# Kernel tuning notes

Measured on AMD Instinct MI355X. Metric: run time of the kernel, lower is better.

The kernel has to match this reference:

```python
import jax, jax.numpy as jnp
import numpy as np

H, W, WS, HEADS = 112, 112, 7, 8
DIM, HID = 512, 2048


def _layernorm(x, g, b, eps=1e-5):
    mu = jnp.mean(x, axis=-1, keepdims=True)
    var = jnp.var(x, axis=-1, keepdims=True)
    return (x - mu) * jax.lax.rsqrt(var + eps) * g + b


def _cpe(x, w, b):
    # depthwise 3x3 conv positional encoding with residual; x: [B, L, C]
    B, L, C = x.shape
    img = x.reshape(B, H, W, C)
    feat = jax.lax.conv_general_dilated(
        img, w, window_strides=(1, 1), padding='SAME',
        dimension_numbers=('NHWC', 'HWIO', 'NHWC'), feature_group_count=C) + b
    return x + feat.reshape(B, L, C)


def _window_partition(x):
    # [B, H, W, C] -> [B*nW, ws*ws, C]
    B, _, _, C = x.shape
    x = x.reshape(B, H // WS, WS, W // WS, WS, C)
    x = jnp.transpose(x, (0, 1, 3, 2, 4, 5))
    return x.reshape(-1, WS * WS, C)


def _window_reverse(xw, B):
    # [B*nW, ws*ws, C] -> [B, H*W, C]
    C = xw.shape[-1]
    x = xw.reshape(B, H // WS, W // WS, WS, WS, C)
    x = jnp.transpose(x, (0, 1, 3, 2, 4, 5))
    return x.reshape(B, H * W, C)


def _attention(x, qkv_w, qkv_b, proj_w, proj_b):
    # x: [nW, N, C]; standard MHA within each window
    nW, N, C = x.shape
    d = C // HEADS
    qkv = x @ qkv_w + qkv_b                      # [nW, N, 3C]
    qkv = qkv.reshape(nW, N, 3, HEADS, d)
    q, k, v = qkv[:, :, 0], qkv[:, :, 1], qkv[:, :, 2]  # [nW, N, h, d]
    scale = d ** -0.5
    attn = jnp.einsum('wqhd,wkhd->whqk', q * scale, k)
    attn = jax.nn.softmax(attn, axis=-1)
    out = jnp.einsum('whqk,wkhd->wqhd', attn, v).reshape(nW, N, C)
    return out @ proj_w + proj_b


def setup_inputs() -> dict:
    key = jax.random.key(0)
    ks = jax.random.split(key, 16)
    s = 0.02
    return {
        'x': jax.random.normal(ks[0], (4, H * W, DIM), jnp.float32),
        'cpe0_w': jax.random.normal(ks[1], (3, 3, 1, DIM), jnp.float32) * s,
        'cpe0_b': jnp.zeros((DIM,), jnp.float32),
        'cpe1_w': jax.random.normal(ks[2], (3, 3, 1, DIM), jnp.float32) * s,
        'cpe1_b': jnp.zeros((DIM,), jnp.float32),
        'ln1_g': jnp.ones((DIM,), jnp.float32),
        'ln1_b': jnp.zeros((DIM,), jnp.float32),
        'ln2_g': jnp.ones((DIM,), jnp.float32),
        'ln2_b': jnp.zeros((DIM,), jnp.float32),
        'qkv_w': jax.random.normal(ks[3], (DIM, 3 * DIM), jnp.float32) * s,
        'qkv_b': jnp.zeros((3 * DIM,), jnp.float32),
        'attn_proj_w': jax.random.normal(ks[4], (DIM, DIM), jnp.float32) * s,
        'attn_proj_b': jnp.zeros((DIM,), jnp.float32),
        'fc1_w': jax.random.normal(ks[5], (DIM, HID), jnp.float32) * s,
        'fc1_b': jnp.zeros((HID,), jnp.float32),
        'fc2_w': jax.random.normal(ks[6], (HID, DIM), jnp.float32) * s,
        'fc2_b': jnp.zeros((DIM,), jnp.float32),
    }


def reference(x, cpe0_w, cpe0_b, cpe1_w, cpe1_b, ln1_g, ln1_b, ln2_g, ln2_b,
              qkv_w, qkv_b, attn_proj_w, attn_proj_b, fc1_w, fc1_b, fc2_w, fc2_b):
    B, L, C = x.shape
    shortcut = _cpe(x, cpe0_w, cpe0_b)                 # CPE #1 (with residual)
    h = _layernorm(shortcut, ln1_g, ln1_b)
    h = _window_partition(h.reshape(B, H, W, C))       # [B*nW, 49, C]
    h = _attention(h, qkv_w, qkv_b, attn_proj_w, attn_proj_b)
    h = _window_reverse(h, B)                          # [B, L, C]
    h = shortcut + h
    h = _cpe(h, cpe1_w, cpe1_b)                        # CPE #2 (with residual)
    m = _layernorm(h, ln2_g, ln2_b)
    m = jax.nn.gelu(m @ fc1_w + fc1_b) @ fc2_w + fc2_b
    return h + m
```

## Files before the change

### kernel.cpp

```cpp
#include <hip/hip_runtime.h>
#include <stdint.h>

#define HH 112
#define WW 112
#define CC 512
#define BB 4
#define LLEN (HH*WW)
#define NTOK (BB*LLEN)
#define NHEADS 8
#define HD 64
#define HIDDEN 2048

typedef __bf16 bf16x8 __attribute__((ext_vector_type(8)));
typedef float f32x4 __attribute__((ext_vector_type(4)));
typedef int i32x8 __attribute__((ext_vector_type(8)));
typedef long i64;

__device__ __forceinline__ unsigned short f2bf(float x) {
  uint32_t u = __float_as_uint(x);
  u += 0x7fffu + ((u >> 16) & 1u);
  return (unsigned short)(u >> 16);
}
__device__ __forceinline__ float bf2f(unsigned short h) {
  return __uint_as_float((uint32_t)h << 16);
}
__device__ __forceinline__ int cvt4_fp8(float a, float b, float c, float d) {
  int r = 0;
  r = __builtin_amdgcn_cvt_pk_fp8_f32(a, b, r, false);
  r = __builtin_amdgcn_cvt_pk_fp8_f32(c, d, r, true);
  return r;
}

__device__ __forceinline__ void gload16(const void* gptr, void* lptr) {
  __builtin_amdgcn_global_load_lds(
      (const __attribute__((address_space(1))) void*)gptr,
      (__attribute__((address_space(3))) void*)lptr,
      16, 0, 0);
}

#define WAITV3() asm volatile("s_waitcnt vmcnt(3)" ::: "memory")
#define WAITV8() asm volatile("s_waitcnt vmcnt(8)" ::: "memory")
#define WAITV0() asm volatile("s_waitcnt vmcnt(0)" ::: "memory")
#define BAR() __builtin_amdgcn_s_barrier()
#define WAITL() do { asm volatile("s_waitcnt lgkmcnt(0)" ::: "memory"); \
                     __builtin_amdgcn_sched_barrier(0); } while (0)

__global__ __launch_bounds__(256) void wtranspose8_kernel(
    const float* __restrict__ w, unsigned char* __restrict__ wt, int K, int N) {
  int idx = blockIdx.x * 256 + threadIdx.x;
  if (idx >= K * N) return;
  int n = idx / K, k = idx - n * K;
  float v = w[(size_t)k * N + n] * 32.f;
  int r = __builtin_amdgcn_cvt_pk_fp8_f32(v, v, 0, false);
  wt[idx] = (unsigned char)r;
}

template <int INBF, int OUTBF>
__global__ __launch_bounds__(256) void cpe_ln_kernel(
    const void* __restrict__ xin, const float* __restrict__ w,
    const float* __restrict__ bias, const float* __restrict__ lng,
    const float* __restrict__ lnb, void* __restrict__ outp,
    unsigned char* __restrict__ ln8) {
  const int wid = threadIdx.x >> 6;
  const int lane = threadIdx.x & 63;
  const int xx = blockIdx.x * 4 + wid;
  const int yy = blockIdx.y;
  const int bb = blockIdx.z;
  const int c = lane * 8;

  float acc[8];
  {
    float4 b0 = *(const float4*)(&bias[c]);
    float4 b1 = *(const float4*)(&bias[c + 4]);
    acc[0] = b0.x; acc[1] = b0.y; acc[2] = b0.z; acc[3] = b0.w;
    acc[4] = b1.x; acc[5] = b1.y; acc[6] = b1.z; acc[7] = b1.w;
  }
  float xv[8];

  #pragma unroll
  for (int ky = 0; ky < 3; ky++) {
    int y = yy + ky - 1;
    bool yok = (unsigned)y < (unsigned)HH;
    #pragma unroll
    for (int kx = 0; kx < 3; kx++) {
      int x2 = xx + kx - 1;
      bool ok = yok && ((unsigned)x2 < (unsigned)WW);
      float v[8];
      if (ok) {
        size_t eo = (((size_t)bb * HH + y) * WW + x2) * CC + c;
        if (INBF) {
          uint4 u = *(const uint4*)(&((const unsigned short*)xin)[eo]);
          v[0] = bf2f((unsigned short)(u.x & 0xffff)); v[1] = bf2f((unsigned short)(u.x >> 16));
          v[2] = bf2f((unsigned short)(u.y & 0xffff)); v[3] = bf2f((unsigned short)(u.y >> 16));
          v[4] = bf2f((unsigned short)(u.z & 0xffff)); v[5] = bf2f((unsigned short)(u.z >> 16));
          v[6] = bf2f((unsigned short)(u.w & 0xffff)); v[7] = bf2f((unsigned short)(u.w >> 16));
        } else {
          float4 a = *(const float4*)(&((const float*)xin)[eo]);
          float4 b = *(const float4*)(&((const float*)xin)[eo + 4]);
          v[0] = a.x; v[1] = a.y; v[2] = a.z; v[3] = a.w;
          v[4] = b.x; v[5] = b.y; v[6] = b.z; v[7] = b.w;
        }
      } else {
        #pragma unroll
        for (int e = 0; e < 8; e++) v[e] = 0.f;
      }
      if (ky == 1 && kx == 1) {
        #pragma unroll
        for (int e = 0; e < 8; e++) xv[e] = v[e];
      }
      float4 w0 = *(const float4*)(&w[(ky * 3 + kx) * CC + c]);
      float4 w1 = *(const float4*)(&w[(ky * 3 + kx) * CC + c + 4]);
      acc[0] = fmaf(v[0], w0.x, acc[0]); acc[1] = fmaf(v[1], w0.y, acc[1]);
      acc[2] = fmaf(v[2], w0.z, acc[2]); acc[3] = fmaf(v[3], w0.w, acc[3]);
      acc[4] = fmaf(v[4], w1.x, acc[4]); acc[5] = fmaf(v[5], w1.y, acc[5]);
      acc[6] = fmaf(v[6], w1.z, acc[6]); acc[7] = fmaf(v[7], w1.w, acc[7]);
    }
  }

  float r[8];
  #pragma unroll
  for (int e = 0; e < 8; e++) r[e] = xv[e] + acc[e];

  const size_t o = (((size_t)bb * HH + yy) * WW + xx) * CC + c;
  if (OUTBF) {
    uint4 pk;
    pk.x = (uint32_t)f2bf(r[0]) | ((uint32_t)f2bf(r[1]) << 16);
    pk.y = (uint32_t)f2bf(r[2]) | ((uint32_t)f2bf(r[3]) << 16);
    pk.z = (uint32_t)f2bf(r[4]) | ((uint32_t)f2bf(r[5]) << 16);
    pk.w = (uint32_t)f2bf(r[6]) | ((uint32_t)f2bf(r[7]) << 16);
    *(uint4*)(&((unsigned short*)outp)[o]) = pk;
  } else {
    float4 r0, r1;
    r0.x = r[0]; r0.y = r[1]; r0.z = r[2]; r0.w = r[3];
    r1.x = r[4]; r1.y = r[5]; r1.z = r[6]; r1.w = r[7];
    *(float4*)(&((float*)outp)[o]) = r0;
    *(float4*)(&((float*)outp)[o + 4]) = r1;
  }

  float s = 0.f, ss = 0.f;
  #pragma unroll
  for (int e = 0; e < 8; e++) { s += r[e]; ss += r[e] * r[e]; }
  #pragma unroll
  for (int of = 32; of; of >>= 1) {
    s += __shfl_xor(s, of, 64);
    ss += __shfl_xor(ss, of, 64);
  }
  float mu = s * (1.f / CC);
  float var = ss * (1.f / CC) - mu * mu;
  float rsd = rsqrtf(var + 1e-5f);
  float4 g0 = *(const float4*)(&lng[c]);
  float4 g1 = *(const float4*)(&lng[c + 4]);
  float4 b0 = *(const float4*)(&lnb[c]);
  float4 b1 = *(const float4*)(&lnb[c + 4]);
  float gv[8] = {g0.x, g0.y, g0.z, g0.w, g1.x, g1.y, g1.z, g1.w};
  float bv[8] = {b0.x, b0.y, b0.z, b0.w, b1.x, b1.y, b1.z, b1.w};
  float ov[8];
  #pragma unroll
  for (int e = 0; e < 8; e++) ov[e] = (r[e] - mu) * rsd * gv[e] + bv[e];
  uint2 pk8;
  pk8.x = (uint32_t)cvt4_fp8(ov[0], ov[1], ov[2], ov[3]);
  pk8.y = (uint32_t)cvt4_fp8(ov[4], ov[5], ov[6], ov[7]);
  *(uint2*)(&ln8[o]) = pk8;
}

#define BM 256
#define BN 128
#define BK8 64

template <int MODE, int K>
__global__ __launch_bounds__(512) void gemm8_kernel(
    const unsigned char* __restrict__ A, const unsigned char* __restrict__ BT,
    const float* __restrict__ bias, const unsigned short* __restrict__ resB,
    unsigned short* __restrict__ outB16, int M, int N) {
  __shared__ unsigned char ldsb[49152];
  int nwg = gridDim.x * gridDim.y;
  int flat = blockIdx.y * gridDim.x + blockIdx.x;
  int swz = (flat & 7) * (nwg >> 3) + (flat >> 3);
  int bx = swz % gridDim.x, by = swz / gridDim.x;
  const int bm = by * BM, bn = bx * BN;
  const int t = threadIdx.x;
  const int wid = t >> 6, lane = t & 63;
  const int wr = wid >> 1, wc = wid & 1;
  const int lr = lane & 15, g = lane >> 4;
  const int swr = (lr >> 1) & 3;
  const int rb0 = (((g >> 1)      ) ^ swr) * 16 + (g & 1) * 8;
  const int rb1 = (((g >> 1) + 2) ^ swr) * 16 + (g & 1) * 8;
  const int srow = t >> 2;
  const int scol = (((t & 3) ^ ((t >> 3) & 3)) & 3) * 16;
  const size_t arow0 = (size_t)(bm + srow) * K + scol;
  const size_t arow1 = (size_t)(bm + 128 + srow) * K + scol;
  const size_t brow  = (size_t)(bn + srow) * K + scol;
  const int ldso = wid * 1024;

#define STG8(b, kt) do { \
    gload16(&A[arow0 + (kt)], ldsb + (b) * 16384 + ldso); \
    gload16(&A[arow1 + (kt)], ldsb + (b) * 16384 + 8192 + ldso); \
    gload16(&BT[brow + (kt)], ldsb + 32768 + (b) * 8192 + ldso); } while (0)

  f32x4 acc[4][4] = {};
  constexpr int nt = K / BK8;

  STG8(0, 0);
  STG8(1, BK8);

  #pragma unroll
  for (int tile = 0; tile < nt - 1; ++tile) {
    WAITV3(); BAR();
    const unsigned char* as = ldsb + (tile & 1) * 16384;
    const unsigned char* bs = ldsb + 32768 + (tile & 1) * 8192;
    i64 af0[4], af1[4], bf0[4], bf1[4];
    #pragma unroll
    for (int i = 0; i < 4; i++) {
      const unsigned char* p = &as[(wr * 64 + i * 16 + lr) * BK8];
      af0[i] = *(const i64*)(p + rb0);
      af1[i] = *(const i64*)(p + rb1);
    }
    #pragma unroll
    for (int j = 0; j < 4; j++) {
      const unsigned char* p = &bs[(wc * 64 + j * 16 + lr) * BK8];
      bf0[j] = *(const i64*)(p + rb0);
      bf1[j] = *(const i64*)(p + rb1);
    }
    WAITL();
    BAR();
    if (tile + 2 < nt) STG8(tile & 1, (tile + 2) * BK8);
    __builtin_amdgcn_s_setprio(1);
    #pragma unroll
    for (int i = 0; i < 4; i++)
      #pragma unroll
      for (int j = 0; j < 4; j++) {
        acc[i][j] = __builtin_amdgcn_mfma_f32_16x16x32_fp8_fp8(af0[i], bf0[j], acc[i][j], 0, 0, 0);
        acc[i][j] = __builtin_amdgcn_mfma_f32_16x16x32_fp8_fp8(af1[i], bf1[j], acc[i][j], 0, 0, 0);
      }
    __builtin_amdgcn_s_setprio(0);
  }
  {
    WAITV0(); BAR();
    const unsigned char* as = ldsb + ((nt - 1) & 1) * 16384;
    const unsigned char* bs = ldsb + 32768 + ((nt - 1) & 1) * 8192;
    i64 af0[4], af1[4], bf0[4], bf1[4];
    #pragma unroll
    for (int i = 0; i < 4; i++) {
      const unsigned char* p = &as[(wr * 64 + i * 16 + lr) * BK8];
      af0[i] = *(const i64*)(p + rb0);
      af1[i] = *(const i64*)(p + rb1);
    }
    #pragma unroll
    for (int j = 0; j < 4; j++) {
      const unsigned char* p = &bs[(wc * 64 + j * 16 + lr) * BK8];
      bf0[j] = *(const i64*)(p + rb0);
      bf1[j] = *(const i64*)(p + rb1);
    }
    WAITL();
    #pragma unroll
    for (int i = 0; i < 4; i++)
      #pragma unroll
      for (int j = 0; j < 4; j++) {
        acc[i][j] = __builtin_amdgcn_mfma_f32_16x16x32_fp8_fp8(af0[i], bf0[j], acc[i][j], 0, 0, 0);
        acc[i][j] = __builtin_amdgcn_mfma_f32_16x16x32_fp8_fp8(af1[i], bf1[j], acc[i][j], 0, 0, 0);
      }
  }
#undef STG8

  {
    const float SC = 0.03125f;
    float* eps = (float*)ldsb;
    const int erow = t >> 3;
    const int ecol0 = (t & 7) * 16;
    const int wrow = wr * 16 + (lane >> 4) * 4;
    const int wcol = wc * 64 + lr;
    const int gr_base = bm + (erow >> 4) * 64 + (erow & 15);
    const int gc0 = bn + ecol0;
    float bv[16];
    #pragma unroll
    for (int c4 = 0; c4 < 4; c4++)
      *(float4*)&bv[c4 * 4] = *(const float4*)&bias[gc0 + c4 * 4];
    #pragma unroll
    for (int i = 0; i < 4; i++) {
      __syncthreads();
      #pragma unroll
      for (int j = 0; j < 4; j++)
        #pragma unroll
        for (int r = 0; r < 4; r++)
          eps[(wrow + r) * 132 + wcol + j * 16] = acc[i][j][r];
      __syncthreads();
      float vv[16];
      #pragma unroll
      for (int c4 = 0; c4 < 4; c4++)
        *(float4*)&vv[c4 * 4] = *(const float4*)&eps[erow * 132 + ecol0 + c4 * 4];
      const size_t off = (size_t)(gr_base + i * 16) * N + gc0;
      uint4 r0 = *(const uint4*)&resB[off];
      uint4 r1 = *(const uint4*)&resB[off + 8];
      unsigned short ob[16];
      const uint32_t* rp = (const uint32_t*)&r0;
      #pragma unroll
      for (int c = 0; c < 8; c++) {
        uint32_t u = rp[c >> 1];
        float rv = bf2f((unsigned short)((c & 1) ? (u >> 16) : (u & 0xffff)));
        ob[c] = f2bf(vv[c] * SC + bv[c] + rv);
      }
      const uint32_t* rp1 = (const uint32_t*)&r1;
      #pragma unroll
      for (int c = 0; c < 8; c++) {
        uint32_t u = rp1[c >> 1];
        float rv = bf2f((unsigned short)((c & 1) ? (u >> 16) : (u & 0xffff)));
        ob[8 + c] = f2bf(vv[8 + c] * SC + bv[8 + c] + rv);
      }
      *(uint4*)&outB16[off]     = *(uint4*)&ob[0];
      *(uint4*)&outB16[off + 8] = *(uint4*)&ob[8];
    }
  }
}

__device__ __forceinline__ i32x8 ld_frag128(const unsigned char* base, int row, int g, int lrm7) {
  const uint4 lo = *(const uint4*)(base + row * 128 + (((2 * g)     ^ lrm7) * 16));
  const uint4 hi = *(const uint4*)(base + row * 128 + (((2 * g + 1) ^ lrm7) * 16));
  i32x8 r;
  r[0] = lo.x; r[1] = lo.y; r[2] = lo.z; r[3] = lo.w;
  r[4] = hi.x; r[5] = hi.y; r[6] = hi.z; r[7] = hi.w;
  return r;
}

template <int MODE, int K>
__global__ __launch_bounds__(256) void gemm8mx_kernel(
    const unsigned char* __restrict__ A, const unsigned char* __restrict__ BT,
    const float* __restrict__ bias, const float* __restrict__ res,
    float* __restrict__ outF, unsigned char* __restrict__ outB8,
    int M, int N) {
  __shared__ unsigned char ldsb[65536];
  const int SCALE1 = 0x7F7F7F7F;
  int nwg = gridDim.x * gridDim.y;
  int flat = blockIdx.y * gridDim.x + blockIdx.x;
  int swz = (flat & 7) * (nwg >> 3) + (flat >> 3);
  int bx = swz % gridDim.x, by = swz / gridDim.x;
  const int bm = by * 128, bn = bx * 128;
  const int t = threadIdx.x;
  const int wid = t >> 6, lane = t & 63;
  const int wr = wid >> 1, wc = wid & 1;
  const int lr = lane & 15, g = lane >> 4, lrm7 = lane & 7;
  const int wq0 = wid * 4096;
  const int scol = (((lane & 7) ^ ((lane >> 3) & 7)) & 7) * 16;
  const size_t aB0 = (size_t)(bm + wid * 32 + ((t >> 3) & 7)) * K + scol;
  const size_t bB0 = (size_t)(bn + wid * 32 + ((t >> 3) & 7)) * K + scol;

#define STGMX(p, kt) do { \
    _Pragma("unroll") for (int q_ = 0; q_ < 4; q_++) { \
      gload16(&A[aB0 + (size_t)q_ * 8 * K + (kt)],  ldsb + (p) * 16384 + wq0 + q_ * 1024); \
      gload16(&BT[bB0 + (size_t)q_ * 8 * K + (kt)], ldsb + 32768 + (p) * 16384 + wq0 + q_ * 1024); \
    } } while (0)

  f32x4 acc[4][4] = {};
  constexpr int npt = K / 128;

  STGMX(0, 0);
  STGMX(1, 128);

  #pragma unroll
  for (int pt = 0; pt < npt - 1; ++pt) {
    WAITV8(); BAR();
    const unsigned char* as = ldsb + (pt & 1) * 16384;
    const unsigned char* bs = ldsb + 32768 + (pt & 1) * 16384;
    i32x8 af[4], bf[4];
    #pragma unroll
    for (int i = 0; i < 4; i++)
      af[i] = ld_frag128(as, wr * 64 + i * 16 + lr, g, lrm7);
    #pragma unroll
    for (int j = 0; j < 4; j++)
      bf[j] = ld_frag128(bs, wc * 64 + j * 16 + lr, g, lrm7);
    WAITL();
    BAR();
    if (pt + 2 < npt) STGMX(pt & 1, (pt + 2) * 128);
    __builtin_amdgcn_s_setprio(1);
    #pragma unroll
    for (int i = 0; i < 4; i++)
      #pragma unroll
      for (int j = 0; j < 4; j++)
        acc[i][j] = __builtin_amdgcn_mfma_scale_f32_16x16x128_f8f6f4(
            af[i], bf[j], acc[i][j], 0, 0, 0, SCALE1, 0, SCALE1);
    __builtin_amdgcn_s_setprio(0);
  }
  {
    WAITV0(); BAR();
    const unsigned char* as = ldsb + ((npt - 1) & 1) * 16384;
    const unsigned char* bs = ldsb + 32768 + ((npt - 1) & 1) * 16384;
    i32x8 af[4], bf[4];
    #pragma unroll
    for (int i = 0; i < 4; i++)
      af[i] = ld_frag128(as, wr * 64 + i * 16 + lr, g, lrm7);
    #pragma unroll
    for (int j = 0; j < 4; j++)
      bf[j] = ld_frag128(bs, wc * 64 + j * 16 + lr, g, lrm7);
    WAITL();
    #pragma unroll
    for (int i = 0; i < 4; i++)
      #pragma unroll
      for (int j = 0; j < 4; j++)
        acc[i][j] = __builtin_amdgcn_mfma_scale_f32_16x16x128_f8f6f4(
            af[i], bf[j], acc[i][j], 0, 0, 0, SCALE1, 0, SCALE1);
  }
#undef STGMX

  {
    const float SC = 0.03125f;
    float* eps = (float*)ldsb;
    const int erow = t >> 2;
    const int cb = (t & 3) * 4;
    float4 bv4[8];
    #pragma unroll
    for (int c = 0; c < 8; c++)
      bv4[c] = *(const float4*)&bias[bn + cb + c * 16];
    #pragma unroll
    for (int p = 0; p < 2; p++) {
      __syncthreads();
      if (wr == p) {
        #pragma unroll
        for (int i = 0; i < 4; i++)
          #pragma unroll
          for (int j = 0; j < 4; j++)
            #pragma unroll
            for (int r = 0; r < 4; r++)
              eps[(i * 16 + g * 4 + r) * 132 + wc * 64 + j * 16 + lr] = acc[i][j][r];
      }
      __syncthreads();
      const size_t rowoff = (size_t)(bm + p * 64 + erow) * N + bn + cb;
      #pragma unroll
      for (int c = 0; c < 8; c++) {
        float4 vv = *(const float4*)&eps[erow * 132 + cb + c * 16];
        float v0 = vv.x * SC + bv4[c].x;
        float v1 = vv.y * SC + bv4[c].y;
        float v2 = vv.z * SC + bv4[c].z;
        float v3 = vv.w * SC + bv4[c].w;
        if (MODE == 1) {
          float4 rv = *(const float4*)&res[rowoff + c * 16];
          float4 ov;
          ov.x = v0 + rv.x; ov.y = v1 + rv.y; ov.z = v2 + rv.z; ov.w = v3 + rv.w;
          *(float4*)&outF[rowoff + c * 16] = ov;
        } else if (MODE == 0) {
          *(uint32_t*)&outB8[rowoff + c * 16] = (uint32_t)cvt4_fp8(v0, v1, v2, v3);
        } else {
          float gv[4];
          float vin[4] = {v0, v1, v2, v3};
          #pragma unroll
          for (int e = 0; e < 4; e++) {
            float v = vin[e];
            float a2 = v * v;
            float w = v * fmaf(a2, -0.1029436f, -2.3024849f);
            float sg = __builtin_amdgcn_rcpf(1.f + __builtin_amdgcn_exp2f(w));
            gv[e] = v * sg;
          }
          *(uint32_t*)&outB8[rowoff + c * 16] = (uint32_t)cvt4_fp8(gv[0], gv[1], gv[2], gv[3]);
        }
      }
    }
  }
}

#define WNS8 72

__global__ __launch_bounds__(64) void attn_mfma8_kernel(
    const unsigned char* __restrict__ qkv, unsigned char* __restrict__ out) {
  __shared__ unsigned char VT[64 * WNS8];
  __shared__ unsigned char Ps[64 * WNS8];
  const int task = blockIdx.x;
  const int win = task >> 3, h = task & 7;
  const int b = win >> 8, wy = (win >> 4) & 15, wx = win & 15;
  const int lane = threadIdx.x;
  const int lr = lane & 15, g = lane >> 4;

  auto tokof = [&](int r) {
    int rr = r > 48 ? 48 : r;
    int y = rr / 7, x2 = rr - y * 7;
    return (size_t)(b * LLEN + (wy * 7 + y) * WW + wx * 7 + x2);
  };

  {
    size_t vbase = tokof(lane) * 1536 + 1024 + h * 64;
    bool valid = lane <= 48;
    #pragma unroll
    for (int c = 0; c < 4; c++) {
      uint4 v = *(const uint4*)(&qkv[vbase + c * 16]);
      const unsigned char* pv = (const unsigned char*)&v;
      #pragma unroll
      for (int e = 0; e < 16; e++)
        VT[(c * 16 + e) * WNS8 + lane] = valid ? pv[e] : (unsigned char)0;
    }
  }

  size_t tok[4];
  #pragma unroll
  for (int i2 = 0; i2 < 4; i2++) tok[i2] = tokof(i2 * 16 + lr);
  i64 Qf[4][2], Kf[4][2];
  #pragma unroll
  for (int i2 = 0; i2 < 4; i2++) {
    size_t base = tok[i2] * 1536 + h * 64 + g * 8;
    #pragma unroll
    for (int ks = 0; ks < 2; ks++) {
      Qf[i2][ks] = *(const i64*)(&qkv[base + ks * 32]);
      Kf[i2][ks] = *(const i64*)(&qkv[base + 512 + ks * 32]);
    }
  }

  f32x4 acc[4][4] = {};
  #pragma unroll
  for (int ks = 0; ks < 2; ks++)
    #pragma unroll
    for (int i2 = 0; i2 < 4; i2++)
      #pragma unroll
      for (int j = 0; j < 4; j++)
        acc[i2][j] = __builtin_amdgcn_mfma_f32_16x16x32_fp8_fp8(Kf[i2][ks], Qf[j][ks], acc[i2][j], 0, 0, 0);

  #pragma unroll
  for (int j = 0; j < 4; j++) {
    float mx = -1e30f;
    #pragma unroll
    for (int i2 = 0; i2 < 4; i2++)
      #pragma unroll
      for (int r = 0; r < 4; r++) {
        int k = 16 * i2 + 4 * g + r;
        mx = fmaxf(mx, (k <= 48) ? acc[i2][j][r] : -1e30f);
      }
    mx = fmaxf(mx, __shfl_xor(mx, 16, 64));
    mx = fmaxf(mx, __shfl_xor(mx, 32, 64));
    float p[4][4];
    float sum = 0.f;
    #pragma unroll
    for (int i2 = 0; i2 < 4; i2++)
      #pragma unroll
      for (int r = 0; r < 4; r++) {
        int k = 16 * i2 + 4 * g + r;
        float e = (k <= 48) ? __expf(0.125f * (acc[i2][j][r] - mx)) : 0.f;
        p[i2][r] = e; sum += e;
      }
    sum += __shfl_xor(sum, 16, 64);
    sum += __shfl_xor(sum, 32, 64);
    float inv = 1.f / sum;
    int q = 16 * j + lr;
    #pragma unroll
    for (int i2 = 0; i2 < 4; i2++) {
      uint32_t w = (uint32_t)cvt4_fp8(p[i2][0] * inv, p[i2][1] * inv,
                                      p[i2][2] * inv, p[i2][3] * inv);
      *(uint32_t*)(&Ps[q * WNS8 + 16 * i2 + 4 * g]) = w;
    }
  }

  __syncthreads();

  f32x4 o[4][4] = {};
  #pragma unroll
  for (int ks = 0; ks < 2; ks++) {
    i64 Pf[4], Vf[4];
    #pragma unroll
    for (int i2 = 0; i2 < 4; i2++)
      Pf[i2] = *(const i64*)(&Ps[(16 * i2 + lr) * WNS8 + ks * 32 + g * 8]);
    #pragma unroll
    for (int j = 0; j < 4; j++)
      Vf[j] = *(const i64*)(&VT[(16 * j + lr) * WNS8 + ks * 32 + g * 8]);
    #pragma unroll
    for (int i2 = 0; i2 < 4; i2++)
      #pragma unroll
      for (int j = 0; j < 4; j++)
        o[i2][j] = __builtin_amdgcn_mfma_f32_16x16x32_fp8_fp8(Pf[i2], Vf[j], o[i2][j], 0, 0, 0);
  }

  #pragma unroll
  for (int i2 = 0; i2 < 4; i2++)
    #pragma unroll
    for (int r = 0; r < 4; r++) {
      int q = 16 * i2 + 4 * g + r;
      if (q <= 48) {
        size_t obase = tokof(q) * 512 + h * 64 + lr;
        #pragma unroll
        for (int j = 0; j < 4; j++) {
          float v = o[i2][j][r];
          int rr = __builtin_amdgcn_cvt_pk_fp8_f32(v, v, 0, false);
          out[obase + 16 * j] = (unsigned char)rr;
        }
      }
    }
}

extern "C" void kernel_launch(void* const* d_in, const int* in_sizes, int n_in,
                              void* d_out, int out_size, void* d_ws, size_t ws_size,
                              hipStream_t stream) {
  const float* x      = (const float*)d_in[0];
  const float* cpe0_w = (const float*)d_in[1];
  const float* cpe0_b = (const float*)d_in[2];
  const float* cpe1_w = (const float*)d_in[3];
  const float* cpe1_b = (const float*)d_in[4];
  const float* ln1_g  = (const float*)d_in[5];
  const float* ln1_b  = (const float*)d_in[6];
  const float* ln2_g  = (const float*)d_in[7];
  const float* ln2_b  = (const float*)d_in[8];
  const float* qkv_w  = (const float*)d_in[9];
  const float* qkv_b  = (const float*)d_in[10];
  const float* proj_w = (const float*)d_in[11];
  const float* proj_b = (const float*)d_in[12];
  const float* fc1_w  = (const float*)d_in[13];
  const float* fc1_b  = (const float*)d_in[14];
  const float* fc2_w  = (const float*)d_in[15];
  const float* fc2_b  = (const float*)d_in[16];
  float* out = (float*)d_out;
  char* ws = (char*)d_ws;

  unsigned char*  qkvwT8 = (unsigned char*)(ws + 0);
  unsigned char*  projwT8 = (unsigned char*)(ws + 1048576);
  unsigned char*  fc1wT8 = (unsigned char*)(ws + 2097152);
  unsigned char*  fc2wT8 = (unsigned char*)(ws + 4194304);
  unsigned short* shortcB = (unsigned short*)(ws + 6291456);
  unsigned char*  lnb8   = (unsigned char*)(ws + 109051904);
  unsigned char*  qkvb8  = (unsigned char*)(ws + 160432128);
  unsigned char*  attnb8 = (unsigned char*)(ws + 314572800);
  unsigned char*  gelub8 = (unsigned char*)(ws + 160432128);
  float* h2 = out;

  wtranspose8_kernel<<<(512 * 1536 + 255) / 256, 256, 0, stream>>>(qkv_w, qkvwT8, 512, 1536);
  wtranspose8_kernel<<<(512 * 512 + 255) / 256, 256, 0, stream>>>(proj_w, projwT8, 512, 512);
  wtranspose8_kernel<<<(512 * 2048 + 255) / 256, 256, 0, stream>>>(fc1_w, fc1wT8, 512, 2048);
  wtranspose8_kernel<<<(2048 * 512 + 255) / 256, 256, 0, stream>>>(fc2_w, fc2wT8, 2048, 512);

  cpe_ln_kernel<0, 1><<<dim3(28, 112, BB), 256, 0, stream>>>(x, cpe0_w, cpe0_b,
      ln1_g, ln1_b, shortcB, lnb8);
  gemm8mx_kernel<0, 512><<<dim3(12, 392), 256, 0, stream>>>(lnb8, qkvwT8, qkv_b, nullptr,
      nullptr, qkvb8, NTOK, 1536);
  attn_mfma8_kernel<<<8192, 64, 0, stream>>>(qkvb8, attnb8);
  gemm8_kernel<3, 512><<<dim3(4, 196), 512, 0, stream>>>(attnb8, projwT8, proj_b,
      shortcB, shortcB, NTOK, 512);
  cpe_ln_kernel<1, 0><<<dim3(28, 112, BB), 256, 0, stream>>>(shortcB, cpe1_w, cpe1_b,
      ln2_g, ln2_b, h2, lnb8);
  gemm8mx_kernel<2, 512><<<dim3(16, 392), 256, 0, stream>>>(lnb8, fc1wT8, fc1_b, nullptr,
      nullptr, gelub8, NTOK, 2048);
  gemm8mx_kernel<1, 2048><<<dim3(4, 392), 256, 0, stream>>>(gelub8, fc2wT8, fc2_b, h2,
      out, nullptr, NTOK, 512);
}
```

Baseline: 536.0 us.

## Use eight waves per block in MX fp8 GEMM with 4x2 wave tiling

Raises the MX fp8 GEMM block from 256 to 512 threads and splits the 128x128 tile across 2x4 waves, each computing 64x32 instead of 64x64. Each thread now issues half as many async global-to-LDS loads, and the wait count is adjusted to match. The epilogue is remapped so each thread handles 16 contiguous columns and writes fp8 output as one 16-byte store. The aim is more latency hiding and wider stores, at the cost of more A-fragment LDS reads per MFMA and heavier barrier synchronisation.

Result: no change. 533.0 us (-0.6%).

```diff
diff --git a/kernel.cpp b/kernel.cpp
--- a/kernel.cpp
+++ b/kernel.cpp
@@ -39,7 +39,7 @@
 }
 
 #define WAITV3() asm volatile("s_waitcnt vmcnt(3)" ::: "memory")
-#define WAITV8() asm volatile("s_waitcnt vmcnt(8)" ::: "memory")
+#define WAITV4() asm volatile("s_waitcnt vmcnt(4)" ::: "memory")
 #define WAITV0() asm volatile("s_waitcnt vmcnt(0)" ::: "memory")
 #define BAR() __builtin_amdgcn_s_barrier()
 #define WAITL() do { asm volatile("s_waitcnt lgkmcnt(0)" ::: "memory"); \
@@ -322,7 +322,7 @@
 }
 
 template <int MODE, int K>
-__global__ __launch_bounds__(256) void gemm8mx_kernel(
+__global__ __launch_bounds__(512) void gemm8mx_kernel(
     const unsigned char* __restrict__ A, const unsigned char* __restrict__ BT,
     const float* __restrict__ bias, const float* __restrict__ res,
     float* __restrict__ outF, unsigned char* __restrict__ outB8,
@@ -336,20 +336,22 @@
   const int bm = by * 128, bn = bx * 128;
   const int t = threadIdx.x;
   const int wid = t >> 6, lane = t & 63;
-  const int wr = wid >> 1, wc = wid & 1;
+  const int wr = wid >> 2, wc = wid & 3;
   const int lr = lane & 15, g = lane >> 4, lrm7 = lane & 7;
-  const int wq0 = wid * 4096;
-  const int scol = (((lane & 7) ^ ((lane >> 3) & 7)) & 7) * 16;
-  const size_t aB0 = (size_t)(bm + wid * 32 + ((t >> 3) & 7)) * K + scol;
-  const size_t bB0 = (size_t)(bn + wid * 32 + ((t >> 3) & 7)) * K + scol;
+  const int srow8 = lane >> 3;
+  const int schunk = ((lane & 7) ^ srow8) * 16;
+  const size_t aBase = (size_t)(bm + wid * 16 + srow8) * K + schunk;
+  const size_t bBase = (size_t)(bn + wid * 16 + srow8) * K + schunk;
+  const size_t row8K = (size_t)8 * K;
+  const int ldsl = wid * 2048;
 
 #define STGMX(p, kt) do { \
-    _Pragma("unroll") for (int q_ = 0; q_ < 4; q_++) { \
-      gload16(&A[aB0 + (size_t)q_ * 8 * K + (kt)],  ldsb + (p) * 16384 + wq0 + q_ * 1024); \
-      gload16(&BT[bB0 + (size_t)q_ * 8 * K + (kt)], ldsb + 32768 + (p) * 16384 + wq0 + q_ * 1024); \
-    } } while (0)
-
-  f32x4 acc[4][4] = {};
+    gload16(&A[aBase + (kt)],          ldsb + (p) * 16384 + ldsl); \
+    gload16(&A[aBase + row8K + (kt)],  ldsb + (p) * 16384 + ldsl + 1024); \
+    gload16(&BT[bBase + (kt)],         ldsb + 32768 + (p) * 16384 + ldsl); \
+    gload16(&BT[bBase + row8K + (kt)], ldsb + 32768 + (p) * 16384 + ldsl + 1024); } while (0)
+
+  f32x4 acc[4][2] = {};
   constexpr int npt = K / 128;
 
   STGMX(0, 0);
@@ -357,16 +359,16 @@
 
   #pragma unroll
   for (int pt = 0; pt < npt - 1; ++pt) {
-    WAITV8(); BAR();
+    WAITV4(); BAR();
     const unsigned char* as = ldsb + (pt & 1) * 16384;
     const unsigned char* bs = ldsb + 32768 + (pt & 1) * 16384;
-    i32x8 af[4], bf[4];
+    i32x8 af[4], bf[2];
     #pragma unroll
     for (int i = 0; i < 4; i++)
       af[i] = ld_frag128(as, wr * 64 + i * 16 + lr, g, lrm7);
     #pragma unroll
-    for (int j = 0; j < 4; j++)
-      bf[j] = ld_frag128(bs, wc * 64 + j * 16 + lr, g, lrm7);
+    for (int j = 0; j < 2; j++)
+      bf[j] = ld_frag128(bs, wc * 32 + j * 16 + lr, g, lrm7);
     WAITL();
     BAR();
     if (pt + 2 < npt) STGMX(pt & 1, (pt + 2) * 128);
@@ -374,7 +376,7 @@
     #pragma unroll
     for (int i = 0; i < 4; i++)
       #pragma unroll
-      for (int j = 0; j < 4; j++)
+      for (int j = 0; j < 2; j++)
         acc[i][j] = __builtin_amdgcn_mfma_scale_f32_16x16x128_f8f6f4(
             af[i], bf[j], acc[i][j], 0, 0, 0, SCALE1, 0, SCALE1);
     __builtin_amdgcn_s_setprio(0);
@@ -383,18 +385,18 @@
     WAITV0(); BAR();
     const unsigned char* as = ldsb + ((npt - 1) & 1) * 16384;
     const unsigned char* bs = ldsb + 32768 + ((npt - 1) & 1) * 16384;
-    i32x8 af[4], bf[4];
+    i32x8 af[4], bf[2];
     #pragma unroll
     for (int i = 0; i < 4; i++)
       af[i] = ld_frag128(as, wr * 64 + i * 16 + lr, g, lrm7);
     #pragma unroll
-    for (int j = 0; j < 4; j++)
-      bf[j] = ld_frag128(bs, wc * 64 + j * 16 + lr, g, lrm7);
+    for (int j = 0; j < 2; j++)
+      bf[j] = ld_frag128(bs, wc * 32 + j * 16 + lr, g, lrm7);
     WAITL();
     #pragma unroll
     for (int i = 0; i < 4; i++)
       #pragma unroll
-      for (int j = 0; j < 4; j++)
+      for (int j = 0; j < 2; j++)
         acc[i][j] = __builtin_amdgcn_mfma_scale_f32_16x16x128_f8f6f4(
             af[i], bf[j], acc[i][j], 0, 0, 0, SCALE1, 0, SCALE1);
   }
@@ -403,12 +405,12 @@
   {
     const float SC = 0.03125f;
     float* eps = (float*)ldsb;
-    const int erow = t >> 2;
-    const int cb = (t & 3) * 4;
-    float4 bv4[8];
-    #pragma unroll
-    for (int c = 0; c < 8; c++)
-      bv4[c] = *(const float4*)&bias[bn + cb + c * 16];
+    const int erow = t >> 3;
+    const int cb = (t & 7) * 16;
+    float4 bv4[4];
+    #pragma unroll
+    for (int c4 = 0; c4 < 4; c4++)
+      bv4[c4] = *(const float4*)&bias[bn + cb + c4 * 4];
     #pragma unroll
     for (int p = 0; p < 2; p++) {
       __syncthreads();
@@ -416,40 +418,51 @@
         #pragma unroll
         for (int i = 0; i < 4; i++)
           #pragma unroll
-          for (int j = 0; j < 4; j++)
+          for (int j = 0; j < 2; j++)
             #pragma unroll
             for (int r = 0; r < 4; r++)
-              eps[(i * 16 + g * 4 + r) * 132 + wc * 64 + j * 16 + lr] = acc[i][j][r];
+              eps[(i * 16 + g * 4 + r) * 132 + wc * 32 + j * 16 + lr] = acc[i][j][r];
       }
       __syncthreads();
       const size_t rowoff = (size_t)(bm + p * 64 + erow) * N + bn + cb;
-      #pragma unroll
-      for (int c = 0; c < 8; c++) {
-        float4 vv = *(const float4*)&eps[erow * 132 + cb + c * 16];
-        float v0 = vv.x * SC + bv4[c].x;
-        float v1 = vv.y * SC + bv4[c].y;
-        float v2 = vv.z * SC + bv4[c].z;
-        float v3 = vv.w * SC + bv4[c].w;
-        if (MODE == 1) {
-          float4 rv = *(const float4*)&res[rowoff + c * 16];
+      if (MODE == 1) {
+        #pragma unroll
+        for (int c4 = 0; c4 < 4; c4++) {
+          float4 vv = *(const float4*)&eps[erow * 132 + cb + c4 * 4];
+          float4 rv = *(const float4*)&res[rowoff + c4 * 4];
           float4 ov;
-          ov.x = v0 + rv.x; ov.y = v1 + rv.y; ov.z = v2 + rv.z; ov.w = v3 + rv.w;
-          *(float4*)&outF[rowoff + c * 16] = ov;
-        } else if (MODE == 0) {
-          *(uint32_t*)&outB8[rowoff + c * 16] = (uint32_t)cvt4_fp8(v0, v1, v2, v3);
-        } else {
-          float gv[4];
-          float vin[4] = {v0, v1, v2, v3};
-          #pragma unroll
-          for (int e = 0; e < 4; e++) {
-            float v = vin[e];
-            float a2 = v * v;
-            float w = v * fmaf(a2, -0.1029436f, -2.3024849f);
-            float sg = __builtin_amdgcn_rcpf(1.f + __builtin_amdgcn_exp2f(w));
-            gv[e] = v * sg;
+          ov.x = vv.x * SC + bv4[c4].x + rv.x;
+          ov.y = vv.y * SC + bv4[c4].y + rv.y;
+          ov.z = vv.z * SC + bv4[c4].z + rv.z;
+          ov.w = vv.w * SC + bv4[c4].w + rv.w;
+          *(float4*)&outF[rowoff + c4 * 4] = ov;
+        }
+      } else {
+        uint32_t ob32[4];
+        #pragma unroll
+        for (int c4 = 0; c4 < 4; c4++) {
+          float4 vv = *(const float4*)&eps[erow * 132 + cb + c4 * 4];
+          float v0 = vv.x * SC + bv4[c4].x;
+          float v1 = vv.y * SC + bv4[c4].y;
+          float v2 = vv.z * SC + bv4[c4].z;
+          float v3 = vv.w * SC + bv4[c4].w;
+          if (MODE == 2) {
+            float vin[4] = {v0, v1, v2, v3};
+            float gvv[4];
+            #pragma unroll
+            for (int e = 0; e < 4; e++) {
+              float v = vin[e];
+              float a2 = v * v;
+              float w = v * fmaf(a2, -0.1029436f, -2.3024849f);
+              float sg = __builtin_amdgcn_rcpf(1.f + __builtin_amdgcn_exp2f(w));
+              gvv[e] = v * sg;
+            }
+            ob32[c4] = (uint32_t)cvt4_fp8(gvv[0], gvv[1], gvv[2], gvv[3]);
+          } else {
+            ob32[c4] = (uint32_t)cvt4_fp8(v0, v1, v2, v3);
           }
-          *(uint32_t*)&outB8[rowoff + c * 16] = (uint32_t)cvt4_fp8(gv[0], gv[1], gv[2], gv[3]);
         }
+        *(uint4*)&outB8[rowoff] = *(uint4*)&ob32[0];
       }
     }
   }
@@ -620,15 +633,15 @@
 
   cpe_ln_kernel<0, 1><<<dim3(28, 112, BB), 256, 0, stream>>>(x, cpe0_w, cpe0_b,
       ln1_g, ln1_b, shortcB, lnb8);
-  gemm8mx_kernel<0, 512><<<dim3(12, 392), 256, 0, stream>>>(lnb8, qkvwT8, qkv_b, nullptr,
+  gemm8mx_kernel<0, 512><<<dim3(12, 392), 512, 0, stream>>>(lnb8, qkvwT8, qkv_b, nullptr,
       nullptr, qkvb8, NTOK, 1536);
   attn_mfma8_kernel<<<8192, 64, 0, stream>>>(qkvb8, attnb8);
   gemm8_kernel<3, 512><<<dim3(4, 196), 512, 0, stream>>>(attnb8, projwT8, proj_b,
       shortcB, shortcB, NTOK, 512);
   cpe_ln_kernel<1, 0><<<dim3(28, 112, BB), 256, 0, stream>>>(shortcB, cpe1_w, cpe1_b,
       ln2_g, ln2_b, h2, lnb8);
-  gemm8mx_kernel<2, 512><<<dim3(16, 392), 256, 0, stream>>>(lnb8, fc1wT8, fc1_b, nullptr,
+  gemm8mx_kernel<2, 512><<<dim3(16, 392), 512, 0, stream>>>(lnb8, fc1wT8, fc1_b, nullptr,
       nullptr, gelub8, NTOK, 2048);
-  gemm8mx_kernel<1, 2048><<<dim3(4, 392), 256, 0, stream>>>(gelub8, fc2wT8, fc2_b, h2,
+  gemm8mx_kernel<1, 2048><<<dim3(4, 392), 512, 0, stream>>>(gelub8, fc2wT8, fc2_b, h2,
       out, nullptr, NTOK, 512);
 }
```
